# Kernel tuning notes

Measured on AMD Instinct MI355X. Metric: run time of the kernel, lower is better.

The kernel has to match this reference:

```python
import jax, jax.numpy as jnp
import numpy as np

EMB = 1024
H = 16
D = EMB // H  # 64
EPS = 1e-5
SM_SCALE = 1.0  # forward default sm_scale=1.0
CAUSAL = True
NEG = -1e30


def _layernorm(t, g, b):
    # LayerNorm over last dim (head_dim), per torch nn.LayerNorm(head_dim)
    m = jnp.mean(t, axis=-1, keepdims=True)
    v = jnp.mean(jnp.square(t - m), axis=-1, keepdims=True)
    return (t - m) * jax.lax.rsqrt(v + EPS) * g + b


def setup_inputs() -> dict:
    key = jax.random.key(0)
    ks = jax.random.split(key, 8)
    N, L = 2, 2048
    x = jax.random.normal(ks[0], (N, L, EMB), dtype=jnp.float32)
    mask = jnp.ones((N, L), dtype=jnp.int32)  # accepted but unused, as in the torch module
    s = 0.02
    Wq = jax.random.normal(ks[1], (EMB, EMB), dtype=jnp.float32) * s
    Wk = jax.random.normal(ks[2], (EMB, EMB), dtype=jnp.float32) * s
    Wv = jax.random.normal(ks[3], (EMB, EMB), dtype=jnp.float32) * s
    Wo = jax.random.normal(ks[4], (EMB, EMB), dtype=jnp.float32) * s
    bo = jnp.zeros((EMB,), dtype=jnp.float32)
    gq = jnp.ones((D,), dtype=jnp.float32)
    bq = jnp.zeros((D,), dtype=jnp.float32)
    gk = jnp.ones((D,), dtype=jnp.float32)
    bk = jnp.zeros((D,), dtype=jnp.float32)
    return {"x": x, "mask": mask, "Wq": Wq, "Wk": Wk, "Wv": Wv,
            "gq": gq, "bq": bq, "gk": gk, "bk": bk, "Wo": Wo, "bo": bo}


def reference(x, mask, Wq, Wk, Wv, gq, bq, gk, bk, Wo, bo):
    N, L, _ = x.shape
    # QKV projections (torch Linear: x @ W.T), split into heads -> [N, H, L, D]
    q = (x @ Wq.T).reshape(N, L, H, D).transpose(0, 2, 1, 3)
    k = (x @ Wk.T).reshape(N, L, H, D).transpose(0, 2, 1, 3)
    v = (x @ Wv.T).reshape(N, L, H, D).transpose(0, 2, 1, 3)
    # fused_q_norm variant: per-head LayerNorm on Q and K (fused into attention kernel)
    q = _layernorm(q, gq, bq)
    k = _layernorm(k, gk, bk)
    scores = jnp.einsum('nhld,nhmd->nhlm', q, k) * SM_SCALE  # [N,H,L,L]
    if CAUSAL:
        causal = jnp.tril(jnp.ones((L, L), dtype=bool))
        scores = jnp.where(causal, scores, NEG)
    attn = jax.nn.softmax(scores, axis=-1)
    out = jnp.einsum('nhlm,nhmd->nhld', attn, v)
    out = out.transpose(0, 2, 1, 3).reshape(N, L, EMB)
    return out @ Wo.T + bo
```

## Files before the change

### kernel.cpp

```cpp
#include <hip/hip_runtime.h>
#include <stdint.h>

typedef unsigned short u16;
typedef u16   u16x4    __attribute__((ext_vector_type(4)));
typedef u16   u16x8    __attribute__((ext_vector_type(8)));
typedef u16x8 u16x8_ma __attribute__((may_alias));
typedef __bf16 bf16x8  __attribute__((ext_vector_type(8)));
typedef float f32x4    __attribute__((ext_vector_type(4)));
typedef f32x4 f32x4_ma __attribute__((may_alias));

#define EMB    1024
#define NHEAD  16
#define HD     64
#define SEQ    2048
#define NBATCH 2
#define ROWS   (NBATCH*SEQ)
#define SATT   72

__device__ __forceinline__ u16 f2b(float f) {
  uint32_t u; __builtin_memcpy(&u, &f, 4);
  u = u + 0x7fffu + ((u >> 16) & 1u);
  return (u16)(u >> 16);
}
__device__ __forceinline__ u16x8 ld8(const u16* p) { return *(const u16x8_ma*)p; }
__device__ __forceinline__ void  st8(u16* p, u16x8 v) { *(u16x8_ma*)p = v; }
__device__ __forceinline__ bf16x8 asbf(u16x8 v) {
  union { u16x8 u; bf16x8 b; } c; c.u = v; return c.b;
}
__device__ __forceinline__ void async_cp16(const u16* g, u16* l) {
  __builtin_amdgcn_global_load_lds(
      (const __attribute__((address_space(1))) void*)g,
      (__attribute__((address_space(3))) void*)l, 16, 0, 0);
}

__global__ __launch_bounds__(256) void cvt_all(
    const float* __restrict__ x,
    const float* __restrict__ w0, const float* __restrict__ w1,
    const float* __restrict__ w2, const float* __restrict__ w3,
    u16* __restrict__ xd, u16* __restrict__ d0, u16* __restrict__ d1,
    u16* __restrict__ d2, u16* __restrict__ d3)
{
  int bid = blockIdx.x;
  const float* s; u16* d; int off;
  if (bid < 4096) { s = x; d = xd; off = bid; }
  else {
    int t = bid - 4096; int m = t >> 10; off = t & 1023;
    switch (m) {
      case 0: s = w0; d = d0; break;
      case 1: s = w1; d = d1; break;
      case 2: s = w2; d = d2; break;
      default: s = w3; d = d3; break;
    }
  }
  size_t i = ((size_t)off * 256 + threadIdx.x) * 4;
  f32x4 v = *(const f32x4_ma*)(s + i);
  u16x4 o;
  #pragma unroll
  for (int j = 0; j < 4; j++) o[j] = f2b(v[j]);
  *(u16x4*)(d + i) = o;
}

template<int AMODE>
__device__ __forceinline__ void gemm_acc_128x128(
    const u16* __restrict__ A, const u16* __restrict__ B,
    int m0, int n0, u16* As, u16* Bs, f32x4 acc[4][4])
{
  const int tid  = threadIdx.x;
  const int lane = tid & 63;
  const int wave = tid >> 6;
  const int wm   = (wave >> 1) * 64;
  const int wn   = (wave & 1) * 64;
  const int ar   = tid >> 2;
  const int ac   = (tid & 3) * 8;
  const int lm   = lane & 15;
  const int lk   = (lane >> 4) * 8;

  #pragma unroll
  for (int i = 0; i < 4; i++)
    #pragma unroll
    for (int j = 0; j < 4; j++)
      #pragma unroll
      for (int e = 0; e < 4; e++) acc[i][j][e] = 0.f;

  for (int k0 = 0; k0 < EMB; k0 += 64) {
    size_t a0[2], a1[2];
    #pragma unroll
    for (int pnl = 0; pnl < 2; pnl++) {
      int kc = k0 + pnl * 32 + ac;
      if (AMODE == 0) {
        a0[pnl] = (size_t)(m0 + ar)      * EMB + kc;
        a1[pnl] = (size_t)(m0 + ar + 64) * EMB + kc;
      } else {
        int h = kc >> 6, d = kc & 63;
        int r0 = m0 + ar, r1 = m0 + ar + 64;
        a0[pnl] = (((size_t)((r0 >> 11) * NHEAD + h)) * SEQ + (r0 & (SEQ-1))) * HD + d;
        a1[pnl] = (((size_t)((r1 >> 11) * NHEAD + h)) * SEQ + (r1 & (SEQ-1))) * HD + d;
      }
    }
    __syncthreads();
    #pragma unroll
    for (int pnl = 0; pnl < 2; pnl++) {
      const int pb = pnl * 4096;
      async_cp16(A + a0[pnl], As + pb + tid * 8);
      async_cp16(A + a1[pnl], As + pb + (tid + 256) * 8);
      async_cp16(B + (size_t)(n0 + ar)      * EMB + k0 + pnl * 32 + ac, Bs + pb + tid * 8);
      async_cp16(B + (size_t)(n0 + ar + 64) * EMB + k0 + pnl * 32 + ac, Bs + pb + (tid + 256) * 8);
    }
    __syncthreads();

    #pragma unroll
    for (int pnl = 0; pnl < 2; pnl++) {
      const int pb = pnl * 4096;
      bf16x8 af[4], bfr[4];
      #pragma unroll
      for (int i = 0; i < 4; i++)
        af[i] = asbf(ld8(As + pb + (wm + i * 16 + lm) * 32 + lk));
      #pragma unroll
      for (int j = 0; j < 4; j++)
        bfr[j] = asbf(ld8(Bs + pb + (wn + j * 16 + lm) * 32 + lk));
      #pragma unroll
      for (int i = 0; i < 4; i++)
        #pragma unroll
        for (int j = 0; j < 4; j++)
          acc[i][j] = __builtin_amdgcn_mfma_f32_16x16x32_bf16(af[i], bfr[j], acc[i][j], 0, 0, 0);
    }
  }
}

__device__ __forceinline__ void epilogue_scatter_ln(
    f32x4 acc[4][4], u16* dst, int m0, int n0, int head_base, int Hdst,
    const float* g, const float* b, int do_ln)
{
  const int lane = threadIdx.x & 63, wave = threadIdx.x >> 6;
  const int wm = (wave >> 1) * 64, wn = (wave & 1) * 64;
  const int lm = lane & 15, quad = lane >> 4;

  float gv[4], bv[4];
  #pragma unroll
  for (int j = 0; j < 4; j++) { gv[j] = g[j * 16 + lm]; bv[j] = b[j * 16 + lm]; }

  #pragma unroll
  for (int i = 0; i < 4; i++)
    #pragma unroll
    for (int r = 0; r < 4; r++) {
      float val[4];
      #pragma unroll
      for (int j = 0; j < 4; j++) val[j] = acc[i][j][r];
      if (do_ln) {
        float s = val[0] + val[1] + val[2] + val[3];
        #pragma unroll
        for (int o = 8; o >= 1; o >>= 1) s += __shfl_xor(s, o, 64);
        float mean = s * (1.f / 64.f);
        float ss = 0.f;
        #pragma unroll
        for (int j = 0; j < 4; j++) { val[j] -= mean; ss += val[j] * val[j]; }
        #pragma unroll
        for (int o = 8; o >= 1; o >>= 1) ss += __shfl_xor(ss, o, 64);
        float inv = rsqrtf(ss * (1.f / 64.f) + 1e-5f);
        #pragma unroll
        for (int j = 0; j < 4; j++) val[j] = val[j] * inv * gv[j] + bv[j];
      }
      int row = m0 + wm + i * 16 + quad * 4 + r;
      int bn = row >> 11, l = row & (SEQ - 1);
      #pragma unroll
      for (int j = 0; j < 4; j++) {
        int col = n0 + wn + j * 16 + lm;
        int hl = (col >> 6) - head_base, d = col & 63;
        dst[(((size_t)(bn * Hdst + hl)) * SEQ + l) * HD + d] = f2b(val[j]);
      }
    }
}

__global__ __launch_bounds__(256) void gemm_qkv(
    const u16* __restrict__ x,
    const u16* __restrict__ Wq, const u16* __restrict__ Wk, const u16* __restrict__ Wv,
    const float* __restrict__ gq, const float* __restrict__ bq,
    const float* __restrict__ gk, const float* __restrict__ bk,
    u16* __restrict__ qd, u16* __restrict__ kb, u16* __restrict__ vb)
{
  __shared__ __align__(16) u16 As[128 * 64];
  __shared__ __align__(16) u16 Bs[128 * 64];
  const u16* W; u16* dst; const float* g; const float* b; int ln;
  if (blockIdx.z == 0)      { W = Wq; dst = qd; g = gq; b = bq; ln = 1; }
  else if (blockIdx.z == 1) { W = Wk; dst = kb; g = gk; b = bk; ln = 1; }
  else                      { W = Wv; dst = vb; g = gq; b = bq; ln = 0; }
  const int m0 = blockIdx.y * 128, n0 = blockIdx.x * 128;
  f32x4 acc[4][4];
  gemm_acc_128x128<0>(x, W, m0, n0, As, Bs, acc);
  epilogue_scatter_ln(acc, dst, m0, n0, 0, NHEAD, g, b, ln);
}

__global__ __launch_bounds__(256) void gemm_q(
    const u16* __restrict__ x, const u16* __restrict__ Wq,
    const float* __restrict__ gq, const float* __restrict__ bq,
    u16* __restrict__ qd)
{
  __shared__ __align__(16) u16 As[128 * 64];
  __shared__ __align__(16) u16 Bs[128 * 64];
  const int m0 = blockIdx.y * 128, n0 = blockIdx.x * 128;
  f32x4 acc[4][4];
  gemm_acc_128x128<0>(x, Wq, m0, n0, As, Bs, acc);
  epilogue_scatter_ln(acc, qd, m0, n0, 0, NHEAD, gq, bq, 1);
}
__global__ __launch_bounds__(256) void gemm_kv(
    const u16* __restrict__ x,
    const u16* __restrict__ Wk, const u16* __restrict__ Wv,
    const float* __restrict__ gk, const float* __restrict__ bk,
    u16* __restrict__ k, u16* __restrict__ v, int head_lo, int hpp)
{
  __shared__ __align__(16) u16 As[128 * 64];
  __shared__ __align__(16) u16 Bs[128 * 64];
  const int m0 = blockIdx.y * 128, n0 = blockIdx.x * 128;
  const u16* W = (blockIdx.z == 0 ? Wk : Wv) + (size_t)head_lo * HD * EMB;
  u16* dst = (blockIdx.z == 0) ? k : v;
  f32x4 acc[4][4];
  gemm_acc_128x128<0>(x, W, m0, n0, As, Bs, acc);
  epilogue_scatter_ln(acc, dst, m0, n0, 0, hpp, gk, bk, blockIdx.z == 0);
}

__global__ __launch_bounds__(256) void attn(
    u16* qd, const u16* __restrict__ K, const u16* __restrict__ V,
    int head_lo, int hpp)
{
  __shared__ __align__(16) u16 Ks[2][64 * SATT];
  __shared__ __align__(16) u16 Vts[2][64 * 64];
  __shared__ __align__(16) u16 Ps[4][16 * SATT];

  const int p = blockIdx.x, hl = blockIdx.y, n = blockIdx.z;
  const int qa = p, qb = 31 - p;
  const int tid = threadIdx.x, lane = tid & 63, wave = tid >> 6;
  const int lm = lane & 15, quad = lane >> 4, lk = quad * 8;
  u16* Qh = qd + ((size_t)(n * NHEAD + head_lo + hl)) * SEQ * HD;
  const u16* Kh = K + ((size_t)(n * hpp + hl)) * SEQ * HD;
  const u16* Vh = V + ((size_t)(n * hpp + hl)) * SEQ * HD;

  const int sr = tid >> 3;
  const int sc = (tid & 7) * 8;
  const int vswz = tid & 7;

  bf16x8 aqA[2], aqB[2];
  #pragma unroll
  for (int ks = 0; ks < 2; ++ks) {
    aqA[ks] = asbf(ld8(Qh + (size_t)(qa * 64 + wave * 16 + lm) * HD + ks * 32 + lk));
    aqB[ks] = asbf(ld8(Qh + (size_t)(qb * 64 + wave * 16 + lm) * HD + ks * 32 + lk));
  }

  u16x8 kr0, kr1, vr0, vr1;
  kr0 = ld8(Kh + (size_t)(sr)      * HD + sc);
  kr1 = ld8(Kh + (size_t)(sr + 32) * HD + sc);
  vr0 = ld8(Vh + (size_t)(sr)      * HD + sc);
  vr1 = ld8(Vh + (size_t)(sr + 32) * HD + sc);
  st8(&Ks[0][sr * SATT + sc], kr0);
  st8(&Ks[0][(sr + 32) * SATT + sc], kr1);
  #pragma unroll
  for (int jj = 0; jj < 8; jj++) {
    int d = sc + jj;
    Vts[0][d * 64 + (((sr >> 3) ^ vswz) * 8) + (sr & 7)]        = vr0[jj];
    Vts[0][d * 64 + ((((sr + 32) >> 3) ^ vswz) * 8) + (sr & 7)] = vr1[jj];
  }
  kr0 = ld8(Kh + (size_t)(64 + sr)      * HD + sc);
  kr1 = ld8(Kh + (size_t)(64 + sr + 32) * HD + sc);
  vr0 = ld8(Vh + (size_t)(64 + sr)      * HD + sc);
  vr1 = ld8(Vh + (size_t)(64 + sr + 32) * HD + sc);
  __syncthreads();

  f32x4 oA[4], oB[4];
  float mA[4], psA[4], mB[4], psB[4];
  #pragma unroll
  for (int j = 0; j < 4; j++)
    #pragma unroll
    for (int e = 0; e < 4; e++) { oA[j][e] = 0.f; oB[j][e] = 0.f; }
  #pragma unroll
  for (int r = 0; r < 4; r++) { mA[r] = -1e30f; psA[r] = 0.f; mB[r] = -1e30f; psB[r] = 0.f; }

  u16* Pw = &Ps[wave][0];

  for (int t = 0; t <= qb; ++t) {
    const int cur = t & 1;
    if (t < qb) {
      const int nb = 1 - cur;
      st8(&Ks[nb][sr * SATT + sc], kr0);
      st8(&Ks[nb][(sr + 32) * SATT + sc], kr1);
      #pragma unroll
      for (int jj = 0; jj < 8; jj++) {
        int d = sc + jj;
        Vts[nb][d * 64 + (((sr >> 3) ^ vswz) * 8) + (sr & 7)]        = vr0[jj];
        Vts[nb][d * 64 + ((((sr + 32) >> 3) ^ vswz) * 8) + (sr & 7)] = vr1[jj];
      }
      if (t + 1 < qb) {
        const size_t base = (size_t)(t + 2) * 64;
        kr0 = ld8(Kh + (base + sr)      * HD + sc);
        kr1 = ld8(Kh + (base + sr + 32) * HD + sc);
        vr0 = ld8(Vh + (base + sr)      * HD + sc);
        vr1 = ld8(Vh + (base + sr + 32) * HD + sc);
      }
    }

    #pragma unroll
    for (int tile = 0; tile < 2; ++tile) {
      if (tile == 1 && t > qa) break;
      const int qx = tile ? qa : qb;
      bf16x8* aq = tile ? aqA : aqB;
      f32x4*  oacc = tile ? oA : oB;
      float*  m_i = tile ? mA : mB;
      float*  psum = tile ? psA : psB;

      f32x4 s[4];
      #pragma unroll
      for (int j = 0; j < 4; j++)
        #pragma unroll
        for (int e = 0; e < 4; e++) s[j][e] = 0.f;
      #pragma unroll
      for (int ks = 0; ks < 2; ++ks)
        #pragma unroll
        for (int j = 0; j < 4; j++) {
          bf16x8 bk = asbf(ld8(&Ks[cur][(j * 16 + lm) * SATT + ks * 32 + lk]));
          s[j] = __builtin_amdgcn_mfma_f32_16x16x32_bf16(aq[ks], bk, s[j], 0, 0, 0);
        }
      if (t == qx) {
        #pragma unroll
        for (int j = 0; j < 4; j++) {
          int col = t * 64 + j * 16 + lm;
          #pragma unroll
          for (int r = 0; r < 4; r++) {
            int row = qx * 64 + wave * 16 + quad * 4 + r;
            if (col > row) s[j][r] = -1e30f;
          }
        }
      }
      float mnew[4], alpha[4], part[4];
      #pragma unroll
      for (int r = 0; r < 4; r++) {
        float mx = fmaxf(fmaxf(s[0][r], s[1][r]), fmaxf(s[2][r], s[3][r]));
        #pragma unroll
        for (int o = 8; o >= 1; o >>= 1) mx = fmaxf(mx, __shfl_xor(mx, o, 64));
        mnew[r] = fmaxf(m_i[r], mx);
        alpha[r] = __expf(m_i[r] - mnew[r]);
        m_i[r] = mnew[r];
        part[r] = 0.f;
      }
      #pragma unroll
      for (int j = 0; j < 4; j++)
        #pragma unroll
        for (int r = 0; r < 4; r++) {
          float pv = __expf(s[j][r] - mnew[r]);
          s[j][r] = pv;
          part[r] += pv;
        }
      #pragma unroll
      for (int r = 0; r < 4; r++) psum[r] = psum[r] * alpha[r] + part[r];
      #pragma unroll
      for (int j = 0; j < 4; j++)
        #pragma unroll
        for (int r = 0; r < 4; r++) oacc[j][r] *= alpha[r];

      #pragma unroll
      for (int j = 0; j < 4; j++)
        #pragma unroll
        for (int r = 0; r < 4; r++)
          Pw[(quad * 4 + r) * SATT + j * 16 + lm] = f2b(s[j][r]);
      __asm__ __volatile__("" ::: "memory");

      #pragma unroll
      for (int ks = 0; ks < 2; ++ks) {
        bf16x8 ap = asbf(ld8(Pw + lm * SATT + ks * 32 + lk));
        #pragma unroll
        for (int j = 0; j < 4; j++) {
          int dg = 2 * j + (lm >> 3);
          int g  = (ks * 4 + quad) ^ (dg & 7);
          bf16x8 bv = asbf(ld8(&Vts[cur][(j * 16 + lm) * 64 + g * 8]));
          oacc[j] = __builtin_amdgcn_mfma_f32_16x16x32_bf16(ap, bv, oacc[j], 0, 0, 0);
        }
      }
    }
    __syncthreads();
  }

  #pragma unroll
  for (int r = 0; r < 4; r++) {
    float sA = psA[r], sB = psB[r];
    #pragma unroll
    for (int o = 8; o >= 1; o >>= 1) { sA += __shfl_xor(sA, o, 64); sB += __shfl_xor(sB, o, 64); }
    float invA = 1.0f / sA, invB = 1.0f / sB;
    int rowA = qa * 64 + wave * 16 + quad * 4 + r;
    int rowB = qb * 64 + wave * 16 + quad * 4 + r;
    #pragma unroll
    for (int j = 0; j < 4; j++) {
      Qh[(size_t)rowB * HD + j * 16 + lm] = f2b(oB[j][r] * invB);
      Qh[(size_t)rowA * HD + j * 16 + lm] = f2b(oA[j][r] * invA);
    }
  }
}

__global__ __launch_bounds__(256) void gemm_out(
    const u16* __restrict__ ao, const u16* __restrict__ Wo,
    const float* __restrict__ bo, float* __restrict__ out)
{
  __shared__ __align__(16) u16 As[64 * 64];
  __shared__ __align__(16) u16 Bs[128 * 64];
  const int m0 = blockIdx.y * 64, n0 = blockIdx.x * 128;
  const int tid  = threadIdx.x;
  const int lane = tid & 63;
  const int wave = tid >> 6;
  const int wm   = (wave >> 1) * 32;
  const int wn   = (wave & 1) * 64;
  const int ar   = tid >> 2;
  const int ac   = (tid & 3) * 8;
  const int lm   = lane & 15;
  const int lk   = (lane >> 4) * 8;

  f32x4 acc[2][4];
  #pragma unroll
  for (int i = 0; i < 2; i++)
    #pragma unroll
    for (int j = 0; j < 4; j++)
      #pragma unroll
      for (int e = 0; e < 4; e++) acc[i][j][e] = 0.f;

  for (int k0 = 0; k0 < EMB; k0 += 64) {
    size_t aoff[2];
    #pragma unroll
    for (int pnl = 0; pnl < 2; pnl++) {
      int kc = k0 + pnl * 32 + ac, h = kc >> 6, d = kc & 63;
      int r0 = m0 + ar;
      aoff[pnl] = (((size_t)((r0 >> 11) * NHEAD + h)) * SEQ + (r0 & (SEQ-1))) * HD + d;
    }
    __syncthreads();
    #pragma unroll
    for (int pnl = 0; pnl < 2; pnl++) {
      async_cp16(ao + aoff[pnl], As + pnl * 2048 + tid * 8);
      async_cp16(Wo + (size_t)(n0 + ar)      * EMB + k0 + pnl * 32 + ac, Bs + pnl * 4096 + tid * 8);
      async_cp16(Wo + (size_t)(n0 + ar + 64) * EMB + k0 + pnl * 32 + ac, Bs + pnl * 4096 + (tid + 256) * 8);
    }
    __syncthreads();

    #pragma unroll
    for (int pnl = 0; pnl < 2; pnl++) {
      bf16x8 af[2], bfr[4];
      #pragma unroll
      for (int i = 0; i < 2; i++)
        af[i] = asbf(ld8(As + pnl * 2048 + (wm + i * 16 + lm) * 32 + lk));
      #pragma unroll
      for (int j = 0; j < 4; j++)
        bfr[j] = asbf(ld8(Bs + pnl * 4096 + (wn + j * 16 + lm) * 32 + lk));
      #pragma unroll
      for (int i = 0; i < 2; i++)
        #pragma unroll
        for (int j = 0; j < 4; j++)
          acc[i][j] = __builtin_amdgcn_mfma_f32_16x16x32_bf16(af[i], bfr[j], acc[i][j], 0, 0, 0);
    }
  }

  const int quad = lane >> 4;
  #pragma unroll
  for (int j = 0; j < 4; j++) {
    int col = n0 + wn + j * 16 + lm;
    float bias = bo[col];
    #pragma unroll
    for (int i = 0; i < 2; i++)
      #pragma unroll
      for (int r = 0; r < 4; r++) {
        int row = m0 + wm + i * 16 + quad * 4 + r;
        out[(size_t)row * EMB + col] = acc[i][j][r] + bias;
      }
  }
}

extern "C" void kernel_launch(void* const* d_in, const int* in_sizes, int n_in,
                              void* d_out, int out_size, void* d_ws, size_t ws_size,
                              hipStream_t stream)
{
  const float* xf  = (const float*)d_in[0];
  const float* Wqf = (const float*)d_in[2];
  const float* Wkf = (const float*)d_in[3];
  const float* Wvf = (const float*)d_in[4];
  const float* gq  = (const float*)d_in[5];
  const float* bq  = (const float*)d_in[6];
  const float* gk  = (const float*)d_in[7];
  const float* bk  = (const float*)d_in[8];
  const float* Wof = (const float*)d_in[9];
  const float* bo  = (const float*)d_in[10];

  const size_t MB = 1u << 20;
  u16* xb  = (u16*)d_ws;
  u16* wqb = xb  + (size_t)ROWS * EMB;
  u16* wkb = wqb + (size_t)EMB * EMB;
  u16* wvb = wkb + (size_t)EMB * EMB;
  u16* wob = wvb + (size_t)EMB * EMB;
  u16* kvbase = wob + (size_t)EMB * EMB;

  size_t avail = (ws_size > 16 * MB) ? ws_size - 16 * MB : 2 * MB;
  int hpp = NHEAD;
  while ((size_t)hpp * MB > avail && hpp > 2) hpp >>= 1;
  const size_t kv_elems = (size_t)hpp * NBATCH * SEQ * HD;
  u16* kbuf = kvbase;
  u16* vbuf = kbuf + kv_elems;

  u16* qd = (u16*)d_in[0];
  float* out = (float*)d_out;

  cvt_all<<<dim3(8192), 256, 0, stream>>>(xf, Wqf, Wkf, Wvf, Wof,
                                          xb, wqb, wkb, wvb, wob);
  if (hpp == NHEAD) {
    gemm_qkv<<<dim3(8, 32, 3), 256, 0, stream>>>(xb, wqb, wkb, wvb,
                                                 gq, bq, gk, bk,
                                                 qd, kbuf, vbuf);
    attn<<<dim3(16, NHEAD, NBATCH), 256, 0, stream>>>(qd, kbuf, vbuf, 0, NHEAD);
  } else {
    gemm_q<<<dim3(8, 32), 256, 0, stream>>>(xb, wqb, gq, bq, qd);
    for (int g = 0; g < NHEAD / hpp; ++g) {
      gemm_kv<<<dim3(hpp / 2, 32, 2), 256, 0, stream>>>(xb, wkb, wvb, gk, bk,
                                                        kbuf, vbuf, g * hpp, hpp);
      attn<<<dim3(16, hpp, NBATCH), 256, 0, stream>>>(qd, kbuf, vbuf, g * hpp, hpp);
    }
  }
  gemm_out<<<dim3(8, 64), 256, 0, stream>>>(qd, wob, bo, out);
}
```

Measured before the change: 229.9 us.

## Load GEMM fragments directly from global memory instead of staging through LDS

Replaces the shared-memory staged 128x128 GEMM main loop with one where each wave loads its MFMA A/B fragments straight from global memory into registers, removing LDS buffers and the two barriers per k-step. The aim is to cut synchronisation and LDS traffic and raise occupancy by freeing shared memory. In exchange, each tile row is now fetched by both waves that share it, so global/L2 traffic roughly doubles, and the 16-byte per-lane loads are strided by the row pitch, which may coalesce poorly. The AMODE head-layout variant of the A operand is dropped.

```diff
diff --git a/kernel.cpp b/kernel.cpp
--- a/kernel.cpp
+++ b/kernel.cpp
@@ -60,18 +60,14 @@
   *(u16x4*)(d + i) = o;
 }
 
-template<int AMODE>
-__device__ __forceinline__ void gemm_acc_128x128(
+__device__ __forceinline__ void gemm_acc_reg_128x128(
     const u16* __restrict__ A, const u16* __restrict__ B,
-    int m0, int n0, u16* As, u16* Bs, f32x4 acc[4][4])
-{
-  const int tid  = threadIdx.x;
-  const int lane = tid & 63;
-  const int wave = tid >> 6;
+    int m0, int n0, f32x4 acc[4][4])
+{
+  const int lane = threadIdx.x & 63;
+  const int wave = threadIdx.x >> 6;
   const int wm   = (wave >> 1) * 64;
   const int wn   = (wave & 1) * 64;
-  const int ar   = tid >> 2;
-  const int ac   = (tid & 3) * 8;
   const int lm   = lane & 15;
   const int lk   = (lane >> 4) * 8;
 
@@ -82,48 +78,26 @@
       #pragma unroll
       for (int e = 0; e < 4; e++) acc[i][j][e] = 0.f;
 
-  for (int k0 = 0; k0 < EMB; k0 += 64) {
-    size_t a0[2], a1[2];
-    #pragma unroll
-    for (int pnl = 0; pnl < 2; pnl++) {
-      int kc = k0 + pnl * 32 + ac;
-      if (AMODE == 0) {
-        a0[pnl] = (size_t)(m0 + ar)      * EMB + kc;
-        a1[pnl] = (size_t)(m0 + ar + 64) * EMB + kc;
-      } else {
-        int h = kc >> 6, d = kc & 63;
-        int r0 = m0 + ar, r1 = m0 + ar + 64;
-        a0[pnl] = (((size_t)((r0 >> 11) * NHEAD + h)) * SEQ + (r0 & (SEQ-1))) * HD + d;
-        a1[pnl] = (((size_t)((r1 >> 11) * NHEAD + h)) * SEQ + (r1 & (SEQ-1))) * HD + d;
-      }
-    }
-    __syncthreads();
-    #pragma unroll
-    for (int pnl = 0; pnl < 2; pnl++) {
-      const int pb = pnl * 4096;
-      async_cp16(A + a0[pnl], As + pb + tid * 8);
-      async_cp16(A + a1[pnl], As + pb + (tid + 256) * 8);
-      async_cp16(B + (size_t)(n0 + ar)      * EMB + k0 + pnl * 32 + ac, Bs + pb + tid * 8);
-      async_cp16(B + (size_t)(n0 + ar + 64) * EMB + k0 + pnl * 32 + ac, Bs + pb + (tid + 256) * 8);
-    }
-    __syncthreads();
-
-    #pragma unroll
-    for (int pnl = 0; pnl < 2; pnl++) {
-      const int pb = pnl * 4096;
-      bf16x8 af[4], bfr[4];
-      #pragma unroll
-      for (int i = 0; i < 4; i++)
-        af[i] = asbf(ld8(As + pb + (wm + i * 16 + lm) * 32 + lk));
-      #pragma unroll
-      for (int j = 0; j < 4; j++)
-        bfr[j] = asbf(ld8(Bs + pb + (wn + j * 16 + lm) * 32 + lk));
-      #pragma unroll
-      for (int i = 0; i < 4; i++)
-        #pragma unroll
-        for (int j = 0; j < 4; j++)
-          acc[i][j] = __builtin_amdgcn_mfma_f32_16x16x32_bf16(af[i], bfr[j], acc[i][j], 0, 0, 0);
-    }
+  const u16* ap[4];
+  const u16* bp[4];
+  #pragma unroll
+  for (int i = 0; i < 4; i++)
+    ap[i] = A + (size_t)(m0 + wm + i * 16 + lm) * EMB + lk;
+  #pragma unroll
+  for (int j = 0; j < 4; j++)
+    bp[j] = B + (size_t)(n0 + wn + j * 16 + lm) * EMB + lk;
+
+  for (int k0 = 0; k0 < EMB; k0 += 32) {
+    bf16x8 af[4], bfr[4];
+    #pragma unroll
+    for (int i = 0; i < 4; i++) af[i]  = asbf(ld8(ap[i] + k0));
+    #pragma unroll
+    for (int j = 0; j < 4; j++) bfr[j] = asbf(ld8(bp[j] + k0));
+    #pragma unroll
+    for (int i = 0; i < 4; i++)
+      #pragma unroll
+      for (int j = 0; j < 4; j++)
+        acc[i][j] = __builtin_amdgcn_mfma_f32_16x16x32_bf16(af[i], bfr[j], acc[i][j], 0, 0, 0);
   }
 }
 
@@ -178,15 +152,13 @@
     const float* __restrict__ gk, const float* __restrict__ bk,
     u16* __restrict__ qd, u16* __restrict__ kb, u16* __restrict__ vb)
 {
-  __shared__ __align__(16) u16 As[128 * 64];
-  __shared__ __align__(16) u16 Bs[128 * 64];
   const u16* W; u16* dst; const float* g; const float* b; int ln;
   if (blockIdx.z == 0)      { W = Wq; dst = qd; g = gq; b = bq; ln = 1; }
   else if (blockIdx.z == 1) { W = Wk; dst = kb; g = gk; b = bk; ln = 1; }
   else                      { W = Wv; dst = vb; g = gq; b = bq; ln = 0; }
   const int m0 = blockIdx.y * 128, n0 = blockIdx.x * 128;
   f32x4 acc[4][4];
-  gemm_acc_128x128<0>(x, W, m0, n0, As, Bs, acc);
+  gemm_acc_reg_128x128(x, W, m0, n0, acc);
   epilogue_scatter_ln(acc, dst, m0, n0, 0, NHEAD, g, b, ln);
 }
 
@@ -195,11 +167,9 @@
     const float* __restrict__ gq, const float* __restrict__ bq,
     u16* __restrict__ qd)
 {
-  __shared__ __align__(16) u16 As[128 * 64];
-  __shared__ __align__(16) u16 Bs[128 * 64];
   const int m0 = blockIdx.y * 128, n0 = blockIdx.x * 128;
   f32x4 acc[4][4];
-  gemm_acc_128x128<0>(x, Wq, m0, n0, As, Bs, acc);
+  gemm_acc_reg_128x128(x, Wq, m0, n0, acc);
   epilogue_scatter_ln(acc, qd, m0, n0, 0, NHEAD, gq, bq, 1);
 }
 __global__ __launch_bounds__(256) void gemm_kv(
@@ -208,13 +178,11 @@
     const float* __restrict__ gk, const float* __restrict__ bk,
     u16* __restrict__ k, u16* __restrict__ v, int head_lo, int hpp)
 {
-  __shared__ __align__(16) u16 As[128 * 64];
-  __shared__ __align__(16) u16 Bs[128 * 64];
   const int m0 = blockIdx.y * 128, n0 = blockIdx.x * 128;
   const u16* W = (blockIdx.z == 0 ? Wk : Wv) + (size_t)head_lo * HD * EMB;
   u16* dst = (blockIdx.z == 0) ? k : v;
   f32x4 acc[4][4];
-  gemm_acc_128x128<0>(x, W, m0, n0, As, Bs, acc);
+  gemm_acc_reg_128x128(x, W, m0, n0, acc);
   epilogue_scatter_ln(acc, dst, m0, n0, 0, hpp, gk, bk, blockIdx.z == 0);
 }
 
```

New measurement: 304.4 us. 1.32x slower.
